# Kernel tuning notes

Measured on AMD Instinct MI355X. Metric: run time of the kernel, lower is better.

The kernel has to match this reference:

```python
import jax, jax.numpy as jnp
import numpy as np

B, J, H, OUT_LEN = 16, 2048, 2048, 128  # seq_len J must equal hidden_dim H
HDIM = H // OUT_LEN  # 16


def setup_inputs() -> dict:
    key = jax.random.key(0)
    k_vec, k_wq, k_wk, k_wv = jax.random.split(key, 4)
    scale = 1.0 / np.sqrt(H)  # keep projections well-scaled (xavier-like)
    return {
        "vec": jax.random.normal(k_vec, (B, J, H), dtype=jnp.float32),
        "wq_w": jax.random.normal(k_wq, (OUT_LEN, H), dtype=jnp.float32) * scale,
        "wq_b": jnp.ones((OUT_LEN,), dtype=jnp.float32),
        "wk_w": jax.random.normal(k_wk, (H, H), dtype=jnp.float32) * scale,
        "wk_b": jnp.ones((H,), dtype=jnp.float32),
        "wv_w": jax.random.normal(k_wv, (HDIM, H), dtype=jnp.float32) * scale,
        "wv_b": jnp.ones((HDIM,), dtype=jnp.float32),
    }


def reference(vec, wq_w, wq_b, wk_w, wk_b, wv_w, wv_b):
    # Projections (nn.Linear: x @ W.T + b)
    q = vec @ wq_w.T + wq_b          # [B, J, out_len]
    k = vec @ wk_w.T + wk_b          # [B, J, H]
    v = vec @ wv_w.T + wv_b          # [B, J, hdim]
    # attn[b, i, h] = sum_j q[b, j, i] * k[b, j, h]  -> [B, out_len, H]
    attn = jnp.einsum('bji,bjk->bij', q, k)
    attn = jax.nn.softmax(jnp.tanh(attn), axis=-1)
    # ret[b, i, d] = sum_j attn[b, i, j] * v[b, j, d]  (requires H == J)
    ret = jnp.einsum('bij,bjk->bik', attn, v)  # [B, out_len, hdim]
    return ret
```

## Files before the change

### kernel.cpp

```cpp
#include <hip/hip_runtime.h>
#include <hip/hip_bf16.h>
#include <math.h>

#define Bn   16
#define Jn   2048
#define Hn   2048
#define OUTn 128
#define HDn  16

#define KC      64
#define NCHUNK  (Hn / KC)
#define B_UNITS 1280
#define WPK_CHUNK_BYTES (2 * B_UNITS * 16)

#define WS_PART1 2048
#define WS_WPK   (WS_PART1 + 256 * 2048)
#define WS_PART  (WS_WPK + NCHUNK * 2 * B_UNITS * 4)

typedef __attribute__((ext_vector_type(8))) short bf16x8_t;
typedef __attribute__((ext_vector_type(4))) float f32x4_t;

typedef __attribute__((address_space(1))) const void gvoid_t;
typedef __attribute__((address_space(3))) void lvoid_t;

__device__ __forceinline__ unsigned short f2bf(float x) {
  unsigned u = __builtin_bit_cast(unsigned, x);
  unsigned r = (u + 0x7fffu + ((u >> 16) & 1u)) >> 16;
  return (unsigned short)r;
}
__device__ __forceinline__ float bf2f(unsigned short h) {
  unsigned u = ((unsigned)h) << 16;
  return __builtin_bit_cast(float, u);
}

__device__ __forceinline__ void cvt8(const float4 u, const float4 v,
                                     bf16x8_t& h, bf16x8_t& l) {
  float x[8] = {u.x, u.y, u.z, u.w, v.x, v.y, v.z, v.w};
#pragma unroll
  for (int i = 0; i < 8; ++i) {
    const unsigned short hi = f2bf(x[i]);
    h[i] = (short)hi;
    l[i] = (short)f2bf(x[i] - bf2f(hi));
  }
}

__global__ __launch_bounds__(256) void prep1_kernel(const float* __restrict__ wk_w,
                                                    const float* __restrict__ wk_b,
                                                    float* __restrict__ ws) {
  const int blk = blockIdx.x;
  const int tid = threadIdx.x;
  if (blk < 256) {
    const int h0 = blk * 8;
    const int c0 = tid * 8;
    float a[8] = {0.f, 0.f, 0.f, 0.f, 0.f, 0.f, 0.f, 0.f};
#pragma unroll
    for (int h = 0; h < 8; ++h) {
      const float* row = wk_w + (size_t)(h0 + h) * Hn + c0;
      const float4 u = *(const float4*)row;
      const float4 v = *(const float4*)(row + 4);
      a[0] += u.x; a[1] += u.y; a[2] += u.z; a[3] += u.w;
      a[4] += v.x; a[5] += v.y; a[6] += v.z; a[7] += v.w;
    }
    float* dst = ws + WS_PART1 + (size_t)blk * Hn + c0;
    *(float4*)dst       = make_float4(a[0], a[1], a[2], a[3]);
    *(float4*)(dst + 4) = make_float4(a[4], a[5], a[6], a[7]);
  } else {
    __shared__ float red[256];
    float s = 0.f;
    for (int h = tid; h < Hn; h += 256) s += wk_b[h];
    red[tid] = s;
    __syncthreads();
    for (int off = 128; off > 0; off >>= 1) {
      if (tid < off) red[tid] += red[tid + off];
      __syncthreads();
    }
    if (tid == 0) ws[0] = red[0];
  }
}

__global__ __launch_bounds__(256) void prep2_kernel(const float* __restrict__ wq_w,
                                                    const float* __restrict__ wv_w,
                                                    const float* __restrict__ ws,
                                                    uint4* __restrict__ wpk) {
  const int id = blockIdx.x * 256 + threadIdx.x;
  const int chunk = id / B_UNITS;
  const int u     = id % B_UNITS;
  const int kblk  = u / 640;
  const int u2    = u % 640;
  const int nt    = u2 >> 6;
  const int g     = (u2 >> 4) & 3;
  const int n16   = u2 & 15;
  const int n     = nt * 16 + n16;
  const int k     = chunk * KC + kblk * 32 + g * 8;

  float x[8];
  if (n < OUTn) {
    const float* s = wq_w + (size_t)n * Hn + k;
#pragma unroll
    for (int i = 0; i < 8; ++i) x[i] = s[i];
  } else if (n < OUTn + HDn) {
    const float* s = wv_w + (size_t)(n - OUTn) * Hn + k;
#pragma unroll
    for (int i = 0; i < 8; ++i) x[i] = s[i];
  } else if (n == OUTn + HDn) {
#pragma unroll
    for (int i = 0; i < 8; ++i) x[i] = 0.f;
    const float* p1 = ws + WS_PART1 + k;
#pragma unroll 8
    for (int p = 0; p < 256; ++p) {
      const float4 a = *(const float4*)p1;
      const float4 b = *(const float4*)(p1 + 4);
      x[0] += a.x; x[1] += a.y; x[2] += a.z; x[3] += a.w;
      x[4] += b.x; x[5] += b.y; x[6] += b.z; x[7] += b.w;
      p1 += Hn;
    }
  } else {
#pragma unroll
    for (int i = 0; i < 8; ++i) x[i] = 0.f;
  }

  unsigned short hi[8], lo[8];
#pragma unroll
  for (int i = 0; i < 8; ++i) {
    hi[i] = f2bf(x[i]);
    lo[i] = f2bf(x[i] - bf2f(hi[i]));
  }
  uint4 uh, ul;
  uh.x = (unsigned)hi[0] | ((unsigned)hi[1] << 16);
  uh.y = (unsigned)hi[2] | ((unsigned)hi[3] << 16);
  uh.z = (unsigned)hi[4] | ((unsigned)hi[5] << 16);
  uh.w = (unsigned)hi[6] | ((unsigned)hi[7] << 16);
  ul.x = (unsigned)lo[0] | ((unsigned)lo[1] << 16);
  ul.y = (unsigned)lo[2] | ((unsigned)lo[3] << 16);
  ul.z = (unsigned)lo[4] | ((unsigned)lo[5] << 16);
  ul.w = (unsigned)lo[6] | ((unsigned)lo[7] << 16);
  wpk[(size_t)(chunk * 2 + 0) * B_UNITS + u] = uh;
  wpk[(size_t)(chunk * 2 + 1) * B_UNITS + u] = ul;
}

__global__ __launch_bounds__(256, 2) void proj_kernel(
    const float* __restrict__ vec,
    const float* __restrict__ wq_b,
    const float* __restrict__ wv_b,
    const float* __restrict__ wsc,
    const uint4* __restrict__ wpk,
    float* __restrict__ part)
{
  __shared__ uint4 Bs[2][2 * B_UNITS];

  const int tid   = threadIdx.x;
  const int lane  = tid & 63;
  const int w     = tid >> 6;
  const int b     = blockIdx.x >> 5;
  const int jt    = blockIdx.x & 31;
  const int j0    = jt * 64;
  const int col16 = lane & 15;
  const int rbase = (lane >> 4) * 4;

  const float* aptr = vec + (size_t)b * Jn * Hn
                    + (size_t)(j0 + w * 16 + col16) * Hn + (lane >> 4) * 8;

  f32x4_t acc[10];
#pragma unroll
  for (int ni = 0; ni < 10; ++ni) acc[ni] = (f32x4_t){0.f, 0.f, 0.f, 0.f};

#define STAGE_B(ch_, buf_)                                                    \
  do {                                                                        \
    const char* gb_ = (const char*)wpk + (size_t)(ch_) * WPK_CHUNK_BYTES +    \
                      (size_t)lane * 16;                                      \
    uint4* bd_ = &Bs[buf_][0];                                                \
    _Pragma("unroll")                                                         \
    for (int i_ = 0; i_ < 10; ++i_) {                                         \
      const int q_ = w + i_ * 4;                                              \
      __builtin_amdgcn_global_load_lds((gvoid_t*)(gb_ + q_ * 1024),           \
                                       (lvoid_t*)(bd_ + q_ * 64), 16, 0, 0);  \
    }                                                                         \
  } while (0)

#define CHUNK_BODY(ch_, buf_, u0, u1, u2, u3, v0_, v1_, v2_, v3_)             \
  do {                                                                        \
    if ((ch_) + 1 < NCHUNK) { STAGE_B((ch_) + 1, (buf_) ^ 1); }               \
    asm volatile("" ::: "memory");     \
    if ((ch_) + 1 < NCHUNK) {                                                 \
      const float* ap_ = aptr + (size_t)((ch_) + 1) * KC;                     \
      v0_ = *(const float4*)(ap_);                                            \
      v1_ = *(const float4*)(ap_ + 4);                                        \
      v2_ = *(const float4*)(ap_ + 32);                                       \
      v3_ = *(const float4*)(ap_ + 36);                                       \
    }                                                                         \
    bf16x8_t ah0_, al0_, ah1_, al1_;                                          \
    cvt8(u0, u1, ah0_, al0_);                                                 \
    cvt8(u2, u3, ah1_, al1_);                                                 \
    const bf16x8_t* B8_ = (const bf16x8_t*)&Bs[buf_][0];                      \
    _Pragma("unroll")                                                         \
    for (int kb_ = 0; kb_ < 2; ++kb_) {                                       \
      const bf16x8_t ah_ = kb_ ? ah1_ : ah0_;                                 \
      const bf16x8_t al_ = kb_ ? al1_ : al0_;                                 \
      _Pragma("unroll")                                                       \
      for (int ni_ = 0; ni_ < 10; ++ni_) {                                    \
        const int idx_ = (kb_ * 10 + ni_) * 64 + lane;                        \
        const bf16x8_t bh_ = B8_[idx_];                                       \
        const bf16x8_t bl_ = B8_[B_UNITS + idx_];                             \
        acc[ni_] = __builtin_amdgcn_mfma_f32_16x16x32_bf16(ah_, bh_, acc[ni_], 0, 0, 0); \
        acc[ni_] = __builtin_amdgcn_mfma_f32_16x16x32_bf16(ah_, bl_, acc[ni_], 0, 0, 0); \
        acc[ni_] = __builtin_amdgcn_mfma_f32_16x16x32_bf16(al_, bh_, acc[ni_], 0, 0, 0); \
      }                                                                       \
    }                                                                         \
    asm volatile("s_waitcnt vmcnt(4)" ::: "memory");  \
    __builtin_amdgcn_s_barrier();                                             \
  } while (0)

  STAGE_B(0, 0);
  asm volatile("" ::: "memory");
  float4 c0 = *(const float4*)(aptr);
  float4 c1 = *(const float4*)(aptr + 4);
  float4 c2 = *(const float4*)(aptr + 32);
  float4 c3 = *(const float4*)(aptr + 36);
  asm volatile("s_waitcnt vmcnt(4)" ::: "memory");
  __builtin_amdgcn_s_barrier();

  float4 n0, n1, n2, n3;
  for (int ch = 0; ch < NCHUNK; ch += 2) {
    CHUNK_BODY(ch,     0, c0, c1, c2, c3, n0, n1, n2, n3);
    CHUNK_BODY(ch + 1, 1, n0, n1, n2, n3, c0, c1, c2, c3);
  }
#undef CHUNK_BODY
#undef STAGE_B

  const float wkb = wsc[0];
  float* q_lds = (float*)Bs;
  float* ks_s  = q_lds + 64 * 132;
  float* vt    = ks_s + 64;
  float* epi   = vt + 64 * 20;

  {
#pragma unroll
    for (int ni = 0; ni < 8; ++ni) {
#pragma unroll
      for (int r = 0; r < 4; ++r) {
        q_lds[(size_t)(w * 16 + rbase + r) * 132 + ni * 16 + col16] = acc[ni][r];
      }
    }
    const float vb_ = wv_b[col16];
#pragma unroll
    for (int r = 0; r < 4; ++r) {
      const int jj = w * 16 + rbase + r;
      vt[jj * 20 + col16] = acc[8][r] + vb_;
    }
    if (col16 == 0) {
#pragma unroll
      for (int r = 0; r < 4; ++r) {
        const int jj = w * 16 + rbase + r;
        ks_s[jj] = acc[9][r] + wkb;
      }
    }
  }
  __syncthreads();

  const int wm   = w >> 1;
  const int wn   = w & 1;
  const int NCOL = wn ? 3 : 5;
  float* epiw = epi + wm * 128 * 18;

#pragma unroll 5
  for (int ni = 0; ni < 5; ++ni) {
    if (ni < NCOL) {
      const float qb = wq_b[(wn * 5 + ni) * 16 + col16];
      float pz = 0.f;
      float po[16];
#pragma unroll
      for (int d = 0; d < 16; ++d) po[d] = 0.f;
#pragma unroll
      for (int mi = 0; mi < 2; ++mi) {
#pragma unroll
        for (int r = 0; r < 4; ++r) {
          const int j = (wm * 2 + mi) * 16 + rbase + r;
          const float ksj = ks_s[j];
          const float4 v0 = *(const float4*)&vt[j * 20];
          const float4 v1 = *(const float4*)&vt[j * 20 + 4];
          const float4 v2 = *(const float4*)&vt[j * 20 + 8];
          const float4 v3 = *(const float4*)&vt[j * 20 + 12];
          const float q   = q_lds[(size_t)j * 132 + (wn * 5 + ni) * 16 + col16] + qb;
          const float e2x = __expf(2.f * q * ksj);
          const float t   = 1.f - 2.f / (e2x + 1.f);
          const float p   = __expf(t);
          pz += p;
          po[0]  += p * v0.x; po[1]  += p * v0.y; po[2]  += p * v0.z; po[3]  += p * v0.w;
          po[4]  += p * v1.x; po[5]  += p * v1.y; po[6]  += p * v1.z; po[7]  += p * v1.w;
          po[8]  += p * v2.x; po[9]  += p * v2.y; po[10] += p * v2.z; po[11] += p * v2.w;
          po[12] += p * v3.x; po[13] += p * v3.y; po[14] += p * v3.z; po[15] += p * v3.w;
        }
      }
      pz += __shfl_xor(pz, 16);
      pz += __shfl_xor(pz, 32);
#pragma unroll
      for (int d = 0; d < 16; ++d) {
        po[d] += __shfl_xor(po[d], 16);
        po[d] += __shfl_xor(po[d], 32);
      }
      if (lane < 16) {
        const int n = (wn * 5 + ni) * 16 + lane;
        epiw[n * 18 + 16] = pz;
#pragma unroll
        for (int d = 0; d < 16; ++d) epiw[n * 18 + d] = po[d];
      }
    }
  }
  __syncthreads();
  float* pout = part + ((size_t)(b * 32 + jt) * 128) * 17;
  for (int idx = tid; idx < 128 * 17; idx += 256) {
    const int row = idx / 17, c = idx % 17;
    pout[idx] = epi[row * 18 + c] + epi[128 * 18 + row * 18 + c];
  }
}

__global__ __launch_bounds__(256) void finalize_kernel(const float* __restrict__ part,
                                                       float* __restrict__ out) {
  const int gid = blockIdx.x * 256 + threadIdx.x;
  const float* p = part + (size_t)(gid >> 7) * 32 * 128 * 17 + (size_t)(gid & 127) * 17;
  float z = 0.f;
  float o[16];
#pragma unroll
  for (int d = 0; d < 16; ++d) o[d] = 0.f;
#pragma unroll 4
  for (int jt = 0; jt < 32; ++jt) {
    const float* pp = p + (size_t)jt * 128 * 17;
    z += pp[16];
#pragma unroll
    for (int d = 0; d < 16; ++d) o[d] += pp[d];
  }
  const float inv = 1.f / z;
  float* dst = out + (size_t)gid * 16;
#pragma unroll
  for (int d = 0; d < 16; ++d) dst[d] = o[d] * inv;
}

extern "C" void kernel_launch(void* const* d_in, const int* in_sizes, int n_in,
                              void* d_out, int out_size, void* d_ws, size_t ws_size,
                              hipStream_t stream) {
  const float* vec  = (const float*)d_in[0];
  const float* wq_w = (const float*)d_in[1];
  const float* wq_b = (const float*)d_in[2];
  const float* wk_w = (const float*)d_in[3];
  const float* wk_b = (const float*)d_in[4];
  const float* wv_w = (const float*)d_in[5];
  const float* wv_b = (const float*)d_in[6];

  float* ws   = (float*)d_ws;
  uint4* wpk  = (uint4*)(ws + WS_WPK);
  float* part = ws + WS_PART;
  float* out  = (float*)d_out;

  prep1_kernel<<<257, 256, 0, stream>>>(wk_w, wk_b, ws);
  prep2_kernel<<<(NCHUNK * B_UNITS) / 256, 256, 0, stream>>>(wq_w, wv_w, ws, wpk);
  proj_kernel<<<Bn * (Jn / 64), 256, 0, stream>>>(vec, wq_b, wv_b, ws, wpk, part);
  finalize_kernel<<<8, 256, 0, stream>>>(part, out);
}
```

Baseline: 449.0 us.

## Switch projection GEMM to 32x32x16 MFMA with split-K across wave pairs

The projection GEMM now uses 32x32x16 bf16 MFMA tiles instead of 16x16x32. Each pair of waves covers 32 rows and splits the K chunk in half, and the packed weight layout is re-indexed to match. Partial accumulators are reduced through LDS before the epilogue writes. The larger tiles should cut LDS B-operand reads per FLOP and the MFMA issue count. In exchange the kernel adds an extra LDS reduction with barriers, and the 5x16 accumulators per lane raise register pressure.

```diff
diff --git a/kernel.cpp b/kernel.cpp
--- a/kernel.cpp
+++ b/kernel.cpp
@@ -19,6 +19,7 @@
 
 typedef __attribute__((ext_vector_type(8))) short bf16x8_t;
 typedef __attribute__((ext_vector_type(4))) float f32x4_t;
+typedef __attribute__((ext_vector_type(16))) float f32x16_t;
 
 typedef __attribute__((address_space(1))) const void gvoid_t;
 typedef __attribute__((address_space(3))) void lvoid_t;
@@ -85,13 +86,12 @@
   const int id = blockIdx.x * 256 + threadIdx.x;
   const int chunk = id / B_UNITS;
   const int u     = id % B_UNITS;
-  const int kblk  = u / 640;
-  const int u2    = u % 640;
-  const int nt    = u2 >> 6;
-  const int g     = (u2 >> 4) & 3;
-  const int n16   = u2 & 15;
-  const int n     = nt * 16 + n16;
-  const int k     = chunk * KC + kblk * 32 + g * 8;
+  const int kstep = u / 320;
+  const int r2    = u % 320;
+  const int nt    = r2 >> 6;
+  const int l     = r2 & 63;
+  const int n     = nt * 32 + (l & 31);
+  const int k     = chunk * KC + kstep * 16 + (l >> 5) * 8;
 
   float x[8];
   if (n < OUTn) {
@@ -151,6 +151,8 @@
   const int tid   = threadIdx.x;
   const int lane  = tid & 63;
   const int w     = tid >> 6;
+  const int wpair = w >> 1;
+  const int whalf = w & 1;
   const int b     = blockIdx.x >> 5;
   const int jt    = blockIdx.x & 31;
   const int j0    = jt * 64;
@@ -158,11 +160,14 @@
   const int rbase = (lane >> 4) * 4;
 
   const float* aptr = vec + (size_t)b * Jn * Hn
-                    + (size_t)(j0 + w * 16 + col16) * Hn + (lane >> 4) * 8;
-
-  f32x4_t acc[10];
-#pragma unroll
-  for (int ni = 0; ni < 10; ++ni) acc[ni] = (f32x4_t){0.f, 0.f, 0.f, 0.f};
+                    + (size_t)(j0 + wpair * 32 + (lane & 31)) * Hn
+                    + whalf * 32 + (lane >> 5) * 8;
+
+  f32x16_t acc[5];
+#pragma unroll
+  for (int ni = 0; ni < 5; ++ni)
+#pragma unroll
+    for (int rg = 0; rg < 16; ++rg) acc[ni][rg] = 0.f;
 
 #define STAGE_B(ch_, buf_)                                                    \
   do {                                                                        \
@@ -185,25 +190,25 @@
       const float* ap_ = aptr + (size_t)((ch_) + 1) * KC;                     \
       v0_ = *(const float4*)(ap_);                                            \
       v1_ = *(const float4*)(ap_ + 4);                                        \
-      v2_ = *(const float4*)(ap_ + 32);                                       \
-      v3_ = *(const float4*)(ap_ + 36);                                       \
+      v2_ = *(const float4*)(ap_ + 16);                                       \
+      v3_ = *(const float4*)(ap_ + 20);                                       \
     }                                                                         \
     bf16x8_t ah0_, al0_, ah1_, al1_;                                          \
     cvt8(u0, u1, ah0_, al0_);                                                 \
     cvt8(u2, u3, ah1_, al1_);                                                 \
     const bf16x8_t* B8_ = (const bf16x8_t*)&Bs[buf_][0];                      \
     _Pragma("unroll")                                                         \
-    for (int kb_ = 0; kb_ < 2; ++kb_) {                                       \
-      const bf16x8_t ah_ = kb_ ? ah1_ : ah0_;                                 \
-      const bf16x8_t al_ = kb_ ? al1_ : al0_;                                 \
+    for (int kl_ = 0; kl_ < 2; ++kl_) {                                       \
+      const bf16x8_t ah_ = kl_ ? ah1_ : ah0_;                                 \
+      const bf16x8_t al_ = kl_ ? al1_ : al0_;                                 \
       _Pragma("unroll")                                                       \
-      for (int ni_ = 0; ni_ < 10; ++ni_) {                                    \
-        const int idx_ = (kb_ * 10 + ni_) * 64 + lane;                        \
+      for (int ni_ = 0; ni_ < 5; ++ni_) {                                     \
+        const int idx_ = ((whalf * 2 + kl_) * 5 + ni_) * 64 + lane;           \
         const bf16x8_t bh_ = B8_[idx_];                                       \
         const bf16x8_t bl_ = B8_[B_UNITS + idx_];                             \
-        acc[ni_] = __builtin_amdgcn_mfma_f32_16x16x32_bf16(ah_, bh_, acc[ni_], 0, 0, 0); \
-        acc[ni_] = __builtin_amdgcn_mfma_f32_16x16x32_bf16(ah_, bl_, acc[ni_], 0, 0, 0); \
-        acc[ni_] = __builtin_amdgcn_mfma_f32_16x16x32_bf16(al_, bh_, acc[ni_], 0, 0, 0); \
+        acc[ni_] = __builtin_amdgcn_mfma_f32_32x32x16_bf16(ah_, bh_, acc[ni_], 0, 0, 0); \
+        acc[ni_] = __builtin_amdgcn_mfma_f32_32x32x16_bf16(ah_, bl_, acc[ni_], 0, 0, 0); \
+        acc[ni_] = __builtin_amdgcn_mfma_f32_32x32x16_bf16(al_, bh_, acc[ni_], 0, 0, 0); \
       }                                                                       \
     }                                                                         \
     asm volatile("s_waitcnt vmcnt(4)" ::: "memory");  \
@@ -214,8 +219,8 @@
   asm volatile("" ::: "memory");
   float4 c0 = *(const float4*)(aptr);
   float4 c1 = *(const float4*)(aptr + 4);
-  float4 c2 = *(const float4*)(aptr + 32);
-  float4 c3 = *(const float4*)(aptr + 36);
+  float4 c2 = *(const float4*)(aptr + 16);
+  float4 c3 = *(const float4*)(aptr + 20);
   asm volatile("s_waitcnt vmcnt(4)" ::: "memory");
   __builtin_amdgcn_s_barrier();
 
@@ -227,31 +232,50 @@
 #undef CHUNK_BODY
 #undef STAGE_B
 
+  __syncthreads();
+  float* lds_f = (float*)Bs;
+  float* redf  = lds_f + 10240;
+  if (whalf == 1) {
+#pragma unroll
+    for (int ni = 0; ni < 5; ++ni)
+#pragma unroll
+      for (int rg = 0; rg < 16; ++rg)
+        redf[wpair * 5120 + (ni * 16 + rg) * 64 + lane] = acc[ni][rg];
+  }
+  __syncthreads();
+
   const float wkb = wsc[0];
-  float* q_lds = (float*)Bs;
+  float* q_lds = lds_f;
   float* ks_s  = q_lds + 64 * 132;
   float* vt    = ks_s + 64;
   float* epi   = vt + 64 * 20;
-
-  {
-#pragma unroll
-    for (int ni = 0; ni < 8; ++ni) {
-#pragma unroll
-      for (int r = 0; r < 4; ++r) {
-        q_lds[(size_t)(w * 16 + rbase + r) * 132 + ni * 16 + col16] = acc[ni][r];
-      }
-    }
-    const float vb_ = wv_b[col16];
-#pragma unroll
-    for (int r = 0; r < 4; ++r) {
-      const int jj = w * 16 + rbase + r;
-      vt[jj * 20 + col16] = acc[8][r] + vb_;
-    }
-    if (col16 == 0) {
-#pragma unroll
-      for (int r = 0; r < 4; ++r) {
-        const int jj = w * 16 + rbase + r;
-        ks_s[jj] = acc[9][r] + wkb;
+  if (whalf == 0) {
+#pragma unroll
+    for (int ni = 0; ni < 5; ++ni)
+#pragma unroll
+      for (int rg = 0; rg < 16; ++rg)
+        acc[ni][rg] += redf[wpair * 5120 + (ni * 16 + rg) * 64 + lane];
+    const int cc = lane & 31;
+    const int jh = 4 * (lane >> 5);
+#pragma unroll
+    for (int nt = 0; nt < 4; ++nt)
+#pragma unroll
+      for (int rg = 0; rg < 16; ++rg) {
+        const int j = wpair * 32 + (rg & 3) + 8 * (rg >> 2) + jh;
+        q_lds[(size_t)j * 132 + nt * 32 + cc] = acc[nt][rg];
+      }
+    if (cc < 16) {
+      const float vb_ = wv_b[cc];
+#pragma unroll
+      for (int rg = 0; rg < 16; ++rg) {
+        const int j = wpair * 32 + (rg & 3) + 8 * (rg >> 2) + jh;
+        vt[j * 20 + cc] = acc[4][rg] + vb_;
+      }
+    } else if (cc == 16) {
+#pragma unroll
+      for (int rg = 0; rg < 16; ++rg) {
+        const int j = wpair * 32 + (rg & 3) + 8 * (rg >> 2) + jh;
+        ks_s[j] = acc[4][rg] + wkb;
       }
     }
   }
```

Measured after the change: 448.1 us. No clear change (-0.2%).
